# Kernel optimization log

Hardware: AMD Instinct MI355X
Metric: run time of the kernel (lower is better)

Reference implementation:

```python
import jax, jax.numpy as jnp
import numpy as np

BATCH = 64
ORIGINAL_DIM = 524288
PROJ_DIM = 8192
C = 4


def setup_inputs() -> dict:
    key = jax.random.key(0)
    k1, k2, k3 = jax.random.split(key, 3)
    x = jax.random.normal(k1, (BATCH, ORIGINAL_DIM), dtype=jnp.float32)
    rand_indices = jax.random.randint(k2, (ORIGINAL_DIM, C), 0, PROJ_DIM, dtype=jnp.int32)
    rand_signs = jax.random.randint(k3, (ORIGINAL_DIM, C), 0, 2, dtype=jnp.int32)
    return {"x": x, "rand_indices": rand_indices, "rand_signs": rand_signs}


def reference(x, rand_indices, rand_signs):
    # SJLT: out[b, rand_indices[d, j]] += x[b, d] * sign[d, j], scaled by 1/sqrt(c)
    B, D = x.shape
    c = rand_indices.shape[1]
    signs = (2 * rand_signs - 1).astype(x.dtype)  # {0,1} -> {-1,+1}
    scale = 1.0 / jnp.sqrt(jnp.asarray(c, dtype=x.dtype))
    out = jnp.zeros((B, PROJ_DIM), dtype=x.dtype)
    for j in range(c):  # small fixed loop over non-zeros per column
        out = out.at[:, rand_indices[:, j]].add(x * signs[:, j])
    return out * scale
```

## Files before the change

### kernel.cpp

```cpp
#include <hip/hip_runtime.h>


constexpr int BATCH = 64;
constexpr int DIM   = 524288;
constexpr int PROJ  = 8192;
constexpr int NENT  = DIM * 4;
constexpr int CAP   = 384;

__device__ __forceinline__ uint32_t f2bf(float f) {
    uint32_t u = __float_as_uint(f);
    return (u + 0x7fffu + ((u >> 16) & 1u)) >> 16;
}

__global__ __launch_bounds__(256) void fused_tx_scatter(
    const float* __restrict__ x, const int* __restrict__ idx,
    const int* __restrict__ sgn, uint32_t* __restrict__ cnt,
    uint32_t* __restrict__ entries, uint32_t* __restrict__ xT)
{
    __shared__ float tile[64][65];
    const int d0 = blockIdx.x * 64;
    const int t  = threadIdx.x;

    const int e = (d0 << 2) + t;
    const int p = idx[e];
    const int s = sgn[e] & 1;

    const int c  = t & 15;
    const int r0 = t >> 4;
    float4 v[4];
#pragma unroll
    for (int it = 0; it < 4; ++it) {
        int b = it * 16 + r0;
        v[it] = *reinterpret_cast<const float4*>(&x[(size_t)b * DIM + d0 + 4 * c]);
    }

    {
        uint32_t dv   = ((uint32_t)(d0 + (t >> 2)) << 1) | (uint32_t)s;
        uint32_t slot = atomicAdd(&cnt[p], 1u);
        entries[(uint32_t)p * (uint32_t)CAP + slot] = dv;
    }

#pragma unroll
    for (int it = 0; it < 4; ++it) {
        int b = it * 16 + r0;
        tile[b][4 * c + 0] = v[it].x;
        tile[b][4 * c + 1] = v[it].y;
        tile[b][4 * c + 2] = v[it].z;
        tile[b][4 * c + 3] = v[it].w;
    }
    __syncthreads();

    const int a  = t & 7;
    const int dr = t >> 3;
#pragma unroll
    for (int pass = 0; pass < 2; ++pass) {
        const int dl = pass * 32 + dr;
        uint4 wv;
        uint32_t* wq = reinterpret_cast<uint32_t*>(&wv);
#pragma unroll
        for (int q = 0; q < 4; ++q) {
            const int k = 4 * a + q;
            uint32_t lo = f2bf(tile[2 * k + 0][dl] * 0.5f);
            uint32_t hi = f2bf(tile[2 * k + 1][dl] * 0.5f);
            wq[q] = lo | (hi << 16);
        }
        *reinterpret_cast<uint4*>(&xT[(size_t)(d0 + dl) * 32 + 4 * a]) = wv;
    }
}

__global__ __launch_bounds__(256) void gather2_kernel(
    const uint32_t* __restrict__ entries, const uint32_t* __restrict__ cnt,
    const uint32_t* __restrict__ xT, float* __restrict__ out)
{
    const int w    = threadIdx.x >> 6;
    const int lane = threadIdx.x & 63;
    const int p    = __builtin_amdgcn_readfirstlane(blockIdx.x * 4 + w);
    const uint32_t n  = __builtin_amdgcn_readfirstlane(cnt[p]);
    const uint32_t e0 = (uint32_t)p * (uint32_t)CAP;

    const int half = lane >> 5;
    const int k    = lane & 31;
    float acc0 = 0.f, acc1 = 0.f;

    uint32_t base = 0;
    for (; base + 8 <= n; base += 8) {
        uint32_t e8[8];
#pragma unroll
        for (int t = 0; t < 8; ++t) e8[t] = entries[e0 + base + t];
#pragma unroll
        for (int t = 0; t < 8; t += 2) {
            uint32_t sel = half ? e8[t + 1] : e8[t];
            uint32_t u = xT[(size_t)(sel >> 1) * 32 + k];
            u ^= (sel & 1u) ? 0u : 0x80008000u;
            acc0 += __uint_as_float(u << 16);
            acc1 += __uint_as_float(u & 0xffff0000u);
        }
    }
    for (; base < n; base += 2) {
        uint32_t eA = entries[e0 + base];
        uint32_t eB = (base + 1 < n) ? entries[e0 + base + 1] : 0u;
        uint32_t sel   = half ? eB : eA;
        bool     valid = (base + (uint32_t)half) < n;
        uint32_t u = 0u;
        if (valid) {
            u = xT[(size_t)(sel >> 1) * 32 + k];
            u ^= (sel & 1u) ? 0u : 0x80008000u;
        }
        acc0 += __uint_as_float(u << 16);
        acc1 += __uint_as_float(u & 0xffff0000u);
    }
    acc0 += __shfl_xor(acc0, 32);
    acc1 += __shfl_xor(acc1, 32);
    if (half == 0) {
        out[(size_t)(2 * k + 0) * PROJ + p] = acc0;
        out[(size_t)(2 * k + 1) * PROJ + p] = acc1;
    }
}

__global__ __launch_bounds__(256) void transpose_hist_kernel(
    const float* __restrict__ x, const int4* __restrict__ idx4,
    uint32_t* __restrict__ xT, uint32_t* __restrict__ cnt)
{
    __shared__ float tile[64][65];
    const int d0   = blockIdx.x * 64;
    const int lane = threadIdx.x & 63;
    const int q    = threadIdx.x >> 6;
#pragma unroll
    for (int r = 0; r < 16; ++r) {
        int b = r * 4 + q;
        tile[b][lane] = x[(size_t)b * DIM + d0 + lane];
    }
    if (threadIdx.x < 64) {
        int4 iv = idx4[d0 + threadIdx.x];
        atomicAdd(&cnt[iv.x], 1u);
        atomicAdd(&cnt[iv.y], 1u);
        atomicAdd(&cnt[iv.z], 1u);
        atomicAdd(&cnt[iv.w], 1u);
    }
    __syncthreads();
    const int k   = threadIdx.x & 31;
    const int dl0 = threadIdx.x >> 5;
#pragma unroll
    for (int pass = 0; pass < 8; ++pass) {
        int dl = pass * 8 + dl0;
        uint32_t lo = f2bf(tile[2 * k + 0][dl] * 0.5f);
        uint32_t hi = f2bf(tile[2 * k + 1][dl] * 0.5f);
        xT[(size_t)(d0 + dl) * 32 + k] = lo | (hi << 16);
    }
}

__global__ __launch_bounds__(256) void scan_kernel(
    const uint32_t* __restrict__ cnt, uint32_t* __restrict__ cur)
{
    __shared__ uint32_t wsum[4];
    const int t    = threadIdx.x;
    const int lane = t & 63;
    uint32_t c[32];
    uint32_t s = 0;
#pragma unroll
    for (int i = 0; i < 32; ++i) { c[i] = cnt[t * 32 + i]; s += c[i]; }
    uint32_t v = s;
#pragma unroll
    for (int off = 1; off < 64; off <<= 1) {
        uint32_t u = __shfl_up(v, off);
        if (lane >= off) v += u;
    }
    if (lane == 63) wsum[t >> 6] = v;
    __syncthreads();
    uint32_t wb = 0;
    for (int w0 = 0; w0 < (t >> 6); ++w0) wb += wsum[w0];
    uint32_t base = wb + v - s;
#pragma unroll
    for (int i = 0; i < 32; ++i) { cur[t * 32 + i] = base; base += c[i]; }
}

__global__ __launch_bounds__(256) void scatter_kernel(
    const int4* __restrict__ idx4, const int4* __restrict__ sgn4,
    uint32_t* __restrict__ cur, uint32_t* __restrict__ entries)
{
    int d = blockIdx.x * 256 + threadIdx.x;
    int4 iv = idx4[d];
    int4 sv = sgn4[d];
    const uint32_t dv = (uint32_t)d << 1;
    uint32_t slot;
    slot = atomicAdd(&cur[iv.x], 1u); entries[slot] = dv | (uint32_t)(sv.x & 1);
    slot = atomicAdd(&cur[iv.y], 1u); entries[slot] = dv | (uint32_t)(sv.y & 1);
    slot = atomicAdd(&cur[iv.z], 1u); entries[slot] = dv | (uint32_t)(sv.z & 1);
    slot = atomicAdd(&cur[iv.w], 1u); entries[slot] = dv | (uint32_t)(sv.w & 1);
}

__global__ __launch_bounds__(256) void gather_kernel(
    const uint32_t* __restrict__ entries, const uint32_t* __restrict__ cnt,
    const uint32_t* __restrict__ endp, const uint32_t* __restrict__ xT,
    float* __restrict__ out)
{
    const int w    = threadIdx.x >> 6;
    const int lane = threadIdx.x & 63;
    const int p    = __builtin_amdgcn_readfirstlane(blockIdx.x * 4 + w);
    const uint32_t n  = __builtin_amdgcn_readfirstlane(cnt[p]);
    const uint32_t e0 = __builtin_amdgcn_readfirstlane(endp[p] - n);

    const int half = lane >> 5;
    const int k    = lane & 31;
    float acc0 = 0.f, acc1 = 0.f;

    uint32_t base = 0;
    for (; base + 8 <= n; base += 8) {
        uint32_t e8[8];
#pragma unroll
        for (int t = 0; t < 8; ++t) e8[t] = entries[e0 + base + t];
#pragma unroll
        for (int t = 0; t < 8; t += 2) {
            uint32_t sel = half ? e8[t + 1] : e8[t];
            uint32_t u = xT[(size_t)(sel >> 1) * 32 + k];
            u ^= (sel & 1u) ? 0u : 0x80008000u;
            acc0 += __uint_as_float(u << 16);
            acc1 += __uint_as_float(u & 0xffff0000u);
        }
    }
    for (; base < n; base += 2) {
        uint32_t eA = entries[e0 + base];
        uint32_t eB = (base + 1 < n) ? entries[e0 + base + 1] : 0u;
        uint32_t sel   = half ? eB : eA;
        bool     valid = (base + (uint32_t)half) < n;
        uint32_t u = 0u;
        if (valid) {
            u = xT[(size_t)(sel >> 1) * 32 + k];
            u ^= (sel & 1u) ? 0u : 0x80008000u;
        }
        acc0 += __uint_as_float(u << 16);
        acc1 += __uint_as_float(u & 0xffff0000u);
    }
    acc0 += __shfl_xor(acc0, 32);
    acc1 += __shfl_xor(acc1, 32);
    if (half == 0) {
        out[(size_t)(2 * k + 0) * PROJ + p] = acc0;
        out[(size_t)(2 * k + 1) * PROJ + p] = acc1;
    }
}

__device__ __forceinline__ void lds_fadd(uint32_t byte_addr, float v) {
    asm volatile("ds_add_f32 %0, %1" :: "v"(byte_addr), "v"(v) : "memory");
}
__device__ __forceinline__ void lds_fadd_off32k(uint32_t byte_addr, float v) {
    asm volatile("ds_add_f32 %0, %1 offset:32768" :: "v"(byte_addr), "v"(v) : "memory");
}

__global__ __launch_bounds__(1024) void sjlt_scatter(
    const float* __restrict__ x, const int4* __restrict__ idx4,
    const int4* __restrict__ sgn4, float* __restrict__ out)
{
    __shared__ float acc[4 * PROJ];
    for (int i = threadIdx.x; i < 4 * PROJ; i += 1024) acc[i] = 0.0f;
    __syncthreads();
    const int row0 = blockIdx.y * 4;
    const int dbeg = blockIdx.x * (DIM / 16);
    const uint32_t accBase = (uint32_t)(uintptr_t)(&acc[0]);
    const float* xr0 = x + (size_t)(row0 + 0) * DIM;
    const float* xr1 = x + (size_t)(row0 + 1) * DIM;
    const float* xr2 = x + (size_t)(row0 + 2) * DIM;
    const float* xr3 = x + (size_t)(row0 + 3) * DIM;
    for (int d = dbeg + (int)threadIdx.x; d < dbeg + DIM / 16; d += 1024) {
        const int4 iv = idx4[d];
        const int4 sv = sgn4[d];
        const uint32_t u0 = __float_as_uint(xr0[d]);
        const uint32_t u1 = __float_as_uint(xr1[d]);
        const uint32_t u2 = __float_as_uint(xr2[d]);
        const uint32_t u3 = __float_as_uint(xr3[d]);
        const int p[4] = {iv.x, iv.y, iv.z, iv.w};
        const int s[4] = {sv.x, sv.y, sv.z, sv.w};
#pragma unroll
        for (int j = 0; j < 4; ++j) {
            const uint32_t flip = (uint32_t)(s[j] ^ 1) << 31;
            const uint32_t a01  = accBase + ((uint32_t)p[j] << 2);
            const uint32_t a23  = a01 + 2u * 32768u;
            lds_fadd        (a01, __uint_as_float(u0 ^ flip));
            lds_fadd_off32k (a01, __uint_as_float(u1 ^ flip));
            lds_fadd        (a23, __uint_as_float(u2 ^ flip));
            lds_fadd_off32k (a23, __uint_as_float(u3 ^ flip));
        }
    }
    __syncthreads();
    for (int i = threadIdx.x; i < 4 * PROJ; i += 1024) {
        const int r  = i >> 13;
        const int pp = i & (PROJ - 1);
        unsafeAtomicAdd(&out[(size_t)(row0 + r) * PROJ + pp], acc[i] * 0.5f);
    }
}

extern "C" void kernel_launch(void* const* d_in, const int* in_sizes, int n_in,
                              void* d_out, int out_size, void* d_ws, size_t ws_size,
                              hipStream_t stream) {
    const float* x   = (const float*)d_in[0];
    const int4*  idx = (const int4*) d_in[1];
    const int4*  sgn = (const int4*) d_in[2];
    float*       out = (float*)d_out;

    const size_t need_new = ((size_t)PROJ + (size_t)PROJ * CAP + (size_t)DIM * 32) * 4;
    const size_t need_old = ((size_t)PROJ + PROJ + NENT + (size_t)DIM * 32) * 4;

    if (ws_size >= need_new) {
        uint32_t* cnt     = (uint32_t*)d_ws;
        uint32_t* entries = cnt + PROJ;
        uint32_t* xT      = entries + (size_t)PROJ * CAP;

        hipMemsetAsync(cnt, 0, PROJ * sizeof(uint32_t), stream);
        fused_tx_scatter<<<DIM / 64, 256, 0, stream>>>(
            x, (const int*)idx, (const int*)sgn, cnt, entries, xT);
        gather2_kernel<<<PROJ / 4, 256, 0, stream>>>(entries, cnt, xT, out);
    } else if (ws_size >= need_old) {
        uint32_t* cnt     = (uint32_t*)d_ws;
        uint32_t* cur     = cnt + PROJ;
        uint32_t* entries = cur + PROJ;
        uint32_t* xT      = entries + NENT;

        hipMemsetAsync(cnt, 0, PROJ * sizeof(uint32_t), stream);
        hipMemsetAsync(entries, 0, (size_t)NENT * sizeof(uint32_t), stream);
        transpose_hist_kernel<<<DIM / 64,  256, 0, stream>>>(x, idx, xT, cnt);
        scan_kernel          <<<1,         256, 0, stream>>>(cnt, cur);
        scatter_kernel       <<<DIM / 256, 256, 0, stream>>>(idx, sgn, cur, entries);
        gather_kernel        <<<PROJ / 4,  256, 0, stream>>>(entries, cnt, cur, xT, out);
    } else {
        hipMemsetAsync(d_out, 0, (size_t)out_size * sizeof(float), stream);
        dim3 grid(16, 16);
        sjlt_scatter<<<grid, 1024, 0, stream>>>(x, idx, sgn, out);
    }
}
```

Measured before the change: 324.6 us.

## Split binning from transpose and bin entries by destination-range blocks

Separates the fused transpose+scatter kernel into a dedicated binning kernel and a plain transpose kernel. Each binning block handles one of eight destination ranges (idx>>10), so atomics and entry writes for a block land in a localized slice of the bucket array, improving cache locality of the scattered writes. The cost is that every idx element is read eight times and one more kernel is launched. Separately, the gather kernel gains a 16-entry unrolled loop for more memory-level parallelism.

```diff
diff --git a/kernel.cpp b/kernel.cpp
--- a/kernel.cpp
+++ b/kernel.cpp
@@ -12,19 +12,13 @@
     return (u + 0x7fffu + ((u >> 16) & 1u)) >> 16;
 }
 
-__global__ __launch_bounds__(256) void fused_tx_scatter(
-    const float* __restrict__ x, const int* __restrict__ idx,
-    const int* __restrict__ sgn, uint32_t* __restrict__ cnt,
-    uint32_t* __restrict__ entries, uint32_t* __restrict__ xT)
+__global__ __launch_bounds__(256) void transpose_kernel(
+    const float* __restrict__ x, uint32_t* __restrict__ xT)
 {
     __shared__ float tile[64][65];
     const int d0 = blockIdx.x * 64;
     const int t  = threadIdx.x;
 
-    const int e = (d0 << 2) + t;
-    const int p = idx[e];
-    const int s = sgn[e] & 1;
-
     const int c  = t & 15;
     const int r0 = t >> 4;
     float4 v[4];
@@ -33,13 +27,6 @@
         int b = it * 16 + r0;
         v[it] = *reinterpret_cast<const float4*>(&x[(size_t)b * DIM + d0 + 4 * c]);
     }
-
-    {
-        uint32_t dv   = ((uint32_t)(d0 + (t >> 2)) << 1) | (uint32_t)s;
-        uint32_t slot = atomicAdd(&cnt[p], 1u);
-        entries[(uint32_t)p * (uint32_t)CAP + slot] = dv;
-    }
-
 #pragma unroll
     for (int it = 0; it < 4; ++it) {
         int b = it * 16 + r0;
@@ -68,7 +55,36 @@
     }
 }
 
-__global__ __launch_bounds__(256) void gather2_kernel(
+__global__ __launch_bounds__(256) void bin_kernel(
+    const int4* __restrict__ idx4, const int4* __restrict__ sgn4,
+    uint32_t* __restrict__ cnt, uint32_t* __restrict__ entries)
+{
+    const int r  = blockIdx.x & 7;
+    const int c0 = (blockIdx.x >> 3) * 256 + threadIdx.x;
+#pragma unroll
+    for (int i = 0; i < 8; ++i) {
+        const int d  = c0 + i * 65536;
+        const int4 iv = idx4[d];
+        const bool m0 = (iv.x >> 10) == r;
+        const bool m1 = (iv.y >> 10) == r;
+        const bool m2 = (iv.z >> 10) == r;
+        const bool m3 = (iv.w >> 10) == r;
+        if (m0 | m1 | m2 | m3) {
+            const int4 sv = sgn4[d];
+            const uint32_t dv = (uint32_t)d << 1;
+            if (m0) { uint32_t sl = atomicAdd(&cnt[iv.x], 1u);
+                      entries[(uint32_t)iv.x * CAP + sl] = dv | (uint32_t)(sv.x & 1); }
+            if (m1) { uint32_t sl = atomicAdd(&cnt[iv.y], 1u);
+                      entries[(uint32_t)iv.y * CAP + sl] = dv | (uint32_t)(sv.y & 1); }
+            if (m2) { uint32_t sl = atomicAdd(&cnt[iv.z], 1u);
+                      entries[(uint32_t)iv.z * CAP + sl] = dv | (uint32_t)(sv.z & 1); }
+            if (m3) { uint32_t sl = atomicAdd(&cnt[iv.w], 1u);
+                      entries[(uint32_t)iv.w * CAP + sl] = dv | (uint32_t)(sv.w & 1); }
+        }
+    }
+}
+
+__global__ __launch_bounds__(256) void gather3_kernel(
     const uint32_t* __restrict__ entries, const uint32_t* __restrict__ cnt,
     const uint32_t* __restrict__ xT, float* __restrict__ out)
 {
@@ -83,6 +99,19 @@
     float acc0 = 0.f, acc1 = 0.f;
 
     uint32_t base = 0;
+    for (; base + 16 <= n; base += 16) {
+        uint32_t e16[16];
+#pragma unroll
+        for (int t = 0; t < 16; ++t) e16[t] = entries[e0 + base + t];
+#pragma unroll
+        for (int t = 0; t < 16; t += 2) {
+            uint32_t sel = half ? e16[t + 1] : e16[t];
+            uint32_t u = xT[(size_t)(sel >> 1) * 32 + k];
+            u ^= (sel & 1u) ? 0u : 0x80008000u;
+            acc0 += __uint_as_float(u << 16);
+            acc1 += __uint_as_float(u & 0xffff0000u);
+        }
+    }
     for (; base + 8 <= n; base += 8) {
         uint32_t e8[8];
 #pragma unroll
@@ -305,9 +334,9 @@
         uint32_t* xT      = entries + (size_t)PROJ * CAP;
 
         hipMemsetAsync(cnt, 0, PROJ * sizeof(uint32_t), stream);
-        fused_tx_scatter<<<DIM / 64, 256, 0, stream>>>(
-            x, (const int*)idx, (const int*)sgn, cnt, entries, xT);
-        gather2_kernel<<<PROJ / 4, 256, 0, stream>>>(entries, cnt, xT, out);
+        bin_kernel      <<<2048,     256, 0, stream>>>(idx, sgn, cnt, entries);
+        transpose_kernel<<<DIM / 64, 256, 0, stream>>>(x, xT);
+        gather3_kernel  <<<PROJ / 4, 256, 0, stream>>>(entries, cnt, xT, out);
     } else if (ws_size >= need_old) {
         uint32_t* cnt     = (uint32_t*)d_ws;
         uint32_t* cur     = cnt + PROJ;
```

After: 454.8 us. 40.1% more time.

## Double-buffer entry loads and coalesce gather output via shared-memory staging

Applied to the files above, without the earlier changes.

The gather kernel now uses 1024-thread blocks that each handle 16 projection columns. Entry indices are software-prefetched into two register buffers, so the next batch of indices loads while the current one's xT gathers run. Results are staged in shared memory and written out as float4 rows instead of strided scalar stores. A new memset clears the whole entries buffer (PROJ*CAP words, about 12.5MB) every call, presumably so the prefetch can safely read past the count, but this adds memory traffic.

```diff
diff --git a/kernel.cpp b/kernel.cpp
--- a/kernel.cpp
+++ b/kernel.cpp
@@ -68,13 +68,28 @@
     }
 }
 
-__global__ __launch_bounds__(256) void gather2_kernel(
+__device__ __forceinline__ void proc8(const uint32_t* __restrict__ e,
+    const uint32_t* __restrict__ xT, int half, int k,
+    float& acc0, float& acc1)
+{
+#pragma unroll
+    for (int t = 0; t < 8; t += 2) {
+        uint32_t sel = half ? e[t + 1] : e[t];
+        uint32_t u = xT[(size_t)(sel >> 1) * 32 + k];
+        u ^= (sel & 1u) ? 0u : 0x80008000u;
+        acc0 += __uint_as_float(u << 16);
+        acc1 += __uint_as_float(u & 0xffff0000u);
+    }
+}
+
+__global__ __launch_bounds__(1024) void gather4_kernel(
     const uint32_t* __restrict__ entries, const uint32_t* __restrict__ cnt,
     const uint32_t* __restrict__ xT, float* __restrict__ out)
 {
+    __shared__ float obuf[64][17];
     const int w    = threadIdx.x >> 6;
     const int lane = threadIdx.x & 63;
-    const int p    = __builtin_amdgcn_readfirstlane(blockIdx.x * 4 + w);
+    const int p    = __builtin_amdgcn_readfirstlane(blockIdx.x * 16 + w);
     const uint32_t n  = __builtin_amdgcn_readfirstlane(cnt[p]);
     const uint32_t e0 = (uint32_t)p * (uint32_t)CAP;
 
@@ -82,19 +97,29 @@
     const int k    = lane & 31;
     float acc0 = 0.f, acc1 = 0.f;
 
+    uint32_t A[8], B[8];
     uint32_t base = 0;
-    for (; base + 8 <= n; base += 8) {
-        uint32_t e8[8];
-#pragma unroll
-        for (int t = 0; t < 8; ++t) e8[t] = entries[e0 + base + t];
-#pragma unroll
-        for (int t = 0; t < 8; t += 2) {
-            uint32_t sel = half ? e8[t + 1] : e8[t];
-            uint32_t u = xT[(size_t)(sel >> 1) * 32 + k];
-            u ^= (sel & 1u) ? 0u : 0x80008000u;
-            acc0 += __uint_as_float(u << 16);
-            acc1 += __uint_as_float(u & 0xffff0000u);
-        }
+    if (n >= 8) {
+#pragma unroll
+        for (int t = 0; t < 8; ++t) A[t] = entries[e0 + t];
+    }
+    for (; base + 24 <= n; base += 16) {
+#pragma unroll
+        for (int t = 0; t < 8; ++t) B[t] = entries[e0 + base + 8 + t];
+        proc8(A, xT, half, k, acc0, acc1);
+#pragma unroll
+        for (int t = 0; t < 8; ++t) A[t] = entries[e0 + base + 16 + t];
+        proc8(B, xT, half, k, acc0, acc1);
+    }
+    if (base + 16 <= n) {
+#pragma unroll
+        for (int t = 0; t < 8; ++t) B[t] = entries[e0 + base + 8 + t];
+        proc8(A, xT, half, k, acc0, acc1);
+        proc8(B, xT, half, k, acc0, acc1);
+        base += 16;
+    } else if (base + 8 <= n) {
+        proc8(A, xT, half, k, acc0, acc1);
+        base += 8;
     }
     for (; base < n; base += 2) {
         uint32_t eA = entries[e0 + base];
@@ -112,8 +137,19 @@
     acc0 += __shfl_xor(acc0, 32);
     acc1 += __shfl_xor(acc1, 32);
     if (half == 0) {
-        out[(size_t)(2 * k + 0) * PROJ + p] = acc0;
-        out[(size_t)(2 * k + 1) * PROJ + p] = acc1;
+        obuf[2 * k + 0][w] = acc0;
+        obuf[2 * k + 1][w] = acc1;
+    }
+    __syncthreads();
+    const int t = threadIdx.x;
+    if (t < 256) {
+        const int b = t >> 2, q = t & 3;
+        float4 v;
+        v.x = obuf[b][4 * q + 0];
+        v.y = obuf[b][4 * q + 1];
+        v.z = obuf[b][4 * q + 2];
+        v.w = obuf[b][4 * q + 3];
+        *reinterpret_cast<float4*>(&out[(size_t)b * PROJ + blockIdx.x * 16 + 4 * q]) = v;
     }
 }
 
@@ -305,9 +341,10 @@
         uint32_t* xT      = entries + (size_t)PROJ * CAP;
 
         hipMemsetAsync(cnt, 0, PROJ * sizeof(uint32_t), stream);
+        hipMemsetAsync(entries, 0, (size_t)PROJ * CAP * sizeof(uint32_t), stream);
         fused_tx_scatter<<<DIM / 64, 256, 0, stream>>>(
             x, (const int*)idx, (const int*)sgn, cnt, entries, xT);
-        gather2_kernel<<<PROJ / 4, 256, 0, stream>>>(entries, cnt, xT, out);
+        gather4_kernel<<<PROJ / 16, 1024, 0, stream>>>(entries, cnt, xT, out);
     } else if (ws_size >= need_old) {
         uint32_t* cnt     = (uint32_t*)d_ws;
         uint32_t* cur     = cnt + PROJ;
```

Measured after the change: 285.8 us. 1.14x faster.
